# Optimization experiments

Measured on AMD Instinct MI355X. Metric: run time of the kernel, lower is better.

Reference implementation:

```python
import jax, jax.numpy as jnp
import numpy as np

N_NODES = 50000
N_EDGES = 800000
D_IN = 128
D_HID = 128
D_OUT = 2


def setup_inputs() -> dict:
    key = jax.random.key(0)
    ks = jax.random.split(key, 8)
    x = jax.random.normal(ks[0], (N_NODES, D_IN), dtype=jnp.float32)
    edge_index = jax.random.randint(ks[1], (2, N_EDGES), 0, N_NODES, dtype=jnp.int64)
    s = 0.05
    W1_l = jax.random.normal(ks[2], (D_HID, D_IN), dtype=jnp.float32) * s
    W1_r = jax.random.normal(ks[3], (D_HID, D_IN), dtype=jnp.float32) * s
    b1 = jax.random.normal(ks[4], (D_HID,), dtype=jnp.float32) * s
    W2_l = jax.random.normal(ks[5], (D_OUT, D_HID), dtype=jnp.float32) * s
    W2_r = jax.random.normal(ks[6], (D_OUT, D_HID), dtype=jnp.float32) * s
    b2 = jax.random.normal(ks[7], (D_OUT,), dtype=jnp.float32) * s
    return {"x": x, "edge_index": edge_index, "W1_l": W1_l, "W1_r": W1_r,
            "b1": b1, "W2_l": W2_l, "W2_r": W2_r, "b2": b2}


def _sage_conv(x, src, dst, W_l, W_r, b):
    # mean-aggregate neighbor features: gather from src, scatter-sum to dst
    n = x.shape[0]
    msg = x[src]                                            # [E, d]
    agg = jax.ops.segment_sum(msg, dst, num_segments=n)      # [n, d]
    cnt = jax.ops.segment_sum(jnp.ones((src.shape[0],), x.dtype), dst,
                              num_segments=n)
    agg = agg / jnp.maximum(cnt, 1.0)[:, None]
    # lin_l(aggregated) + lin_r(self) + bias  (PyG SAGEConv with root_weight)
    return agg @ W_l.T + x @ W_r.T + b


def reference(x, edge_index, W1_l, W1_r, b1, W2_l, W2_r, b2):
    src, dst = edge_index[0], edge_index[1]
    h = _sage_conv(x, src, dst, W1_l, W1_r, b1)
    h = jax.nn.relu(h)
    out = _sage_conv(h, src, dst, W2_l, W2_r, b2)
    return out
```

## Files before the change

kernel.cpp:

```cpp
#include <hip/hip_runtime.h>

#define N_NODES 50000
#define N_EDGES 800000

typedef __bf16 bf16_8 __attribute__((ext_vector_type(8)));
typedef float  f32_4  __attribute__((ext_vector_type(4)));


__global__ void prep_deg_kernel(const float* __restrict__ W1l, const float* __restrict__ W1r,
                                __bf16* __restrict__ Wt, const float* __restrict__ x,
                                __bf16* __restrict__ xb, const int* __restrict__ dst,
                                int* __restrict__ deg_p, int* __restrict__ edge_pos) {
    int b = blockIdx.x;
    if (b < 3125) {
        int t = b * 256 + threadIdx.x;
        int d = dst[t];
        int pos = atomicAdd(&deg_p[d * 16], 1);
        int node = t >> 4, c8 = t & 15;
        const float4* xp = (const float4*)(x + node * 128 + c8 * 8);
        float4 v0 = xp[0], v1 = xp[1];
        bf16_8 o;
        o[0] = (__bf16)v0.x; o[1] = (__bf16)v0.y; o[2] = (__bf16)v0.z; o[3] = (__bf16)v0.w;
        o[4] = (__bf16)v1.x; o[5] = (__bf16)v1.y; o[6] = (__bf16)v1.z; o[7] = (__bf16)v1.w;
        *(bf16_8*)(xb + t * 8) = o;
        edge_pos[t] = pos;
    } else {
        int t = (b - 3125) * 256 + threadIdx.x;
        int n = t >> 8, k = t & 255;
        float v = (k < 128) ? W1l[n * 128 + k] : W1r[n * 128 + (k - 128)];
        Wt[t] = (__bf16)v;
    }
}

__global__ void scan_block_kernel(const int* __restrict__ deg_p, int* __restrict__ rowptr,
                                  int* __restrict__ degc, int* __restrict__ bsum) {
    __shared__ int s[256];
    int i = blockIdx.x * 256 + threadIdx.x;
    int v = (i < N_NODES) ? deg_p[i * 16] : 0;
    if (i < N_NODES) degc[i] = v;
    s[threadIdx.x] = v;
    __syncthreads();
    #pragma unroll
    for (int off = 1; off < 256; off <<= 1) {
        int t = (threadIdx.x >= off) ? s[threadIdx.x - off] : 0;
        __syncthreads();
        s[threadIdx.x] += t;
        __syncthreads();
    }
    if (i < N_NODES) rowptr[i] = s[threadIdx.x] - v;
    if (threadIdx.x == 255) bsum[blockIdx.x] = s[255];
}

__global__ void scan_bsum_kernel(const int* __restrict__ bsum, int* __restrict__ boff) {
    __shared__ int s[256];
    int tid = threadIdx.x;
    int v = (tid < 196) ? bsum[tid] : 0;
    s[tid] = v;
    __syncthreads();
    #pragma unroll
    for (int off = 1; off < 256; off <<= 1) {
        int t = (tid >= off) ? s[tid - off] : 0;
        __syncthreads();
        s[tid] += t;
        __syncthreads();
    }
    boff[tid] = s[tid] - v;
}

__global__ void fill_csr_kernel(const int* __restrict__ src, const int* __restrict__ dst,
                                const int* __restrict__ rowptr, const int* __restrict__ boff,
                                const int* __restrict__ edge_pos, int* __restrict__ csr) {
    int e = blockIdx.x * 256 + threadIdx.x;
    int d = dst[e];
    csr[rowptr[d] + boff[d >> 8] + edge_pos[e]] = src[e];
}

#define LDA 264
__global__ __launch_bounds__(256) void gather_gemm_kernel(
    const int* __restrict__ rowptr, const int* __restrict__ boff,
    const int* __restrict__ degc, const int* __restrict__ csr,
    const __bf16* __restrict__ xb, const __bf16* __restrict__ Wt,
    const float* __restrict__ b1, const float* __restrict__ W2l,
    const float* __restrict__ W2r, float* __restrict__ y, float* __restrict__ z)
{
    __shared__ __bf16 As[16 * LDA];
    __shared__ float4 sp[4][16];

    const int i0 = blockIdx.x * 16;
    const int tid = threadIdx.x;
    const int row = tid >> 4, c8 = tid & 15;
    const int gi = i0 + row;

    bf16_8 sv = *(const bf16_8*)(xb + gi * 128 + c8 * 8);
    *(bf16_8*)(&As[row * LDA + 128 + c8 * 8]) = sv;

    {
        int beg = rowptr[gi] + boff[gi >> 8];
        int n = degc[gi];
        float acc[8] = {};
        int j = 0;
        for (; j + 8 <= n; j += 8) {
            int idx[8];
            #pragma unroll
            for (int u = 0; u < 8; ++u) idx[u] = csr[beg + j + u];
            bf16_8 vv[8];
            #pragma unroll
            for (int u = 0; u < 8; ++u)
                vv[u] = *(const bf16_8*)(xb + idx[u] * 128 + c8 * 8);
            #pragma unroll
            for (int u = 0; u < 8; ++u) {
                float s01 = (float)vv[0][u] + (float)vv[1][u];
                float s23 = (float)vv[2][u] + (float)vv[3][u];
                float s45 = (float)vv[4][u] + (float)vv[5][u];
                float s67 = (float)vv[6][u] + (float)vv[7][u];
                acc[u] += (s01 + s23) + (s45 + s67);
            }
        }
        for (; j + 2 <= n; j += 2) {
            int s0 = csr[beg + j], s1 = csr[beg + j + 1];
            bf16_8 v0 = *(const bf16_8*)(xb + s0 * 128 + c8 * 8);
            bf16_8 v1 = *(const bf16_8*)(xb + s1 * 128 + c8 * 8);
            #pragma unroll
            for (int u = 0; u < 8; ++u) acc[u] += (float)v0[u] + (float)v1[u];
        }
        if (j < n) {
            int s0 = csr[beg + j];
            bf16_8 v0 = *(const bf16_8*)(xb + s0 * 128 + c8 * 8);
            #pragma unroll
            for (int u = 0; u < 8; ++u) acc[u] += (float)v0[u];
        }
        float inv = 1.0f / fmaxf((float)n, 1.0f);
        bf16_8 o;
        #pragma unroll
        for (int u = 0; u < 8; ++u) o[u] = (__bf16)(acc[u] * inv);
        *(bf16_8*)(&As[row * LDA + c8 * 8]) = o;
    }
    __syncthreads();

    const int wv = tid >> 6, lane = tid & 63;
    const int mr = lane & 15, q = lane >> 4;
    const int n0 = wv * 2, n1 = wv * 2 + 1;

    f32_4 acc0 = (f32_4){0.f,0.f,0.f,0.f}, acc1 = (f32_4){0.f,0.f,0.f,0.f};
    #pragma unroll
    for (int ks = 0; ks < 8; ++ks) {
        bf16_8 a  = *(const bf16_8*)(&As[mr * LDA + ks * 32 + q * 8]);
        bf16_8 b0 = *(const bf16_8*)(Wt + (n0 * 16 + mr) * 256 + ks * 32 + q * 8);
        bf16_8 bb = *(const bf16_8*)(Wt + (n1 * 16 + mr) * 256 + ks * 32 + q * 8);
        acc0 = __builtin_amdgcn_mfma_f32_16x16x32_bf16(a, b0, acc0, 0, 0, 0);
        acc1 = __builtin_amdgcn_mfma_f32_16x16x32_bf16(a, bb, acc1, 0, 0, 0);
    }

    float py0[4] = {}, py1[4] = {}, pz0[4] = {}, pz1[4] = {};
    #pragma unroll
    for (int ntl = 0; ntl < 2; ++ntl) {
        int col = (wv * 2 + ntl) * 16 + mr;
        f32_4 a = ntl ? acc1 : acc0;
        float bb  = b1[col];
        float wl0 = W2l[col], wl1 = W2l[128 + col];
        float wr0 = W2r[col], wr1 = W2r[128 + col];
        #pragma unroll
        for (int r = 0; r < 4; ++r) {
            float hv = fmaxf(a[r] + bb, 0.f);
            py0[r] += hv * wl0; py1[r] += hv * wl1;
            pz0[r] += hv * wr0; pz1[r] += hv * wr1;
        }
    }
    #pragma unroll
    for (int off = 1; off < 16; off <<= 1) {
        #pragma unroll
        for (int r = 0; r < 4; ++r) {
            py0[r] += __shfl_xor(py0[r], off);
            py1[r] += __shfl_xor(py1[r], off);
            pz0[r] += __shfl_xor(pz0[r], off);
            pz1[r] += __shfl_xor(pz1[r], off);
        }
    }
    if (mr < 4) {
        int r = mr;
        sp[wv][q * 4 + r] = make_float4(py0[r], py1[r], pz0[r], pz1[r]);
    }
    __syncthreads();

    if (tid < 16) {
        float4 a0 = sp[0][tid], a1 = sp[1][tid], a2 = sp[2][tid], a3 = sp[3][tid];
        ((float2*)y)[i0 + tid] = make_float2(a0.x + a1.x + a2.x + a3.x,
                                             a0.y + a1.y + a2.y + a3.y);
        ((float2*)z)[i0 + tid] = make_float2(a0.z + a1.z + a2.z + a3.z,
                                             a0.w + a1.w + a2.w + a3.w);
    }
}

__global__ void final_kernel(const int* __restrict__ rowptr, const int* __restrict__ boff,
                             const int* __restrict__ degc, const int* __restrict__ csr,
                             const float* __restrict__ y, const float* __restrict__ z,
                             const float* __restrict__ b2, float* __restrict__ out) {
    int t = blockIdx.x * 256 + threadIdx.x;
    int node = t >> 2, p = t & 3;
    if (node >= N_NODES) return;
    int beg = rowptr[node] + boff[node >> 8], n = degc[node];
    float a0 = 0.f, a1 = 0.f;
    for (int j = p; j < n; j += 4) {
        float2 v = ((const float2*)y)[csr[beg + j]];
        a0 += v.x; a1 += v.y;
    }
    a0 += __shfl_xor(a0, 1); a1 += __shfl_xor(a1, 1);
    a0 += __shfl_xor(a0, 2); a1 += __shfl_xor(a1, 2);
    if (p == 0) {
        float inv = 1.0f / fmaxf((float)n, 1.0f);
        float2 zz = ((const float2*)z)[node];
        ((float2*)out)[node] = make_float2(a0 * inv + zz.x + b2[0],
                                           a1 * inv + zz.y + b2[1]);
    }
}

extern "C" void kernel_launch(void* const* d_in, const int* in_sizes, int n_in,
                              void* d_out, int out_size, void* d_ws, size_t ws_size,
                              hipStream_t stream) {
    const float* x   = (const float*)d_in[0];
    const int*   ei  = (const int*)  d_in[1];
    const float* W1l = (const float*)d_in[2];
    const float* W1r = (const float*)d_in[3];
    const float* b1  = (const float*)d_in[4];
    const float* W2l = (const float*)d_in[5];
    const float* W2r = (const float*)d_in[6];
    const float* b2  = (const float*)d_in[7];
    float* out = (float*)d_out;
    const int* src = ei;
    const int* dst = ei + N_EDGES;

    char* ws = (char*)d_ws;
    int*    deg_p    = (int*)   (ws + 0);
    int*    boff     = (int*)   (ws + 0);
    int*    edge_pos = (int*)   (ws + 3200000);
    int*    rowptr   = (int*)   (ws + 6400000);
    int*    degc     = (int*)   (ws + 6600192);
    int*    bsum     = (int*)   (ws + 6800384);
    int*    csr      = (int*)   (ws + 6801408);
    __bf16* xb       = (__bf16*)(ws + 10001408);
    float*  y        = (float*) (ws + 35601408);
    float*  z        = (float*) (ws + 36001408);
    __bf16* Wt       = (__bf16*)(ws + 36401408);

    hipMemsetAsync(deg_p, 0, 3200000, stream);
    prep_deg_kernel<<<3253, 256, 0, stream>>>(W1l, W1r, Wt, x, xb, dst, deg_p, edge_pos);
    scan_block_kernel<<<196, 256, 0, stream>>>(deg_p, rowptr, degc, bsum);
    scan_bsum_kernel<<<1, 256, 0, stream>>>(bsum, boff);
    fill_csr_kernel<<<3125, 256, 0, stream>>>(src, dst, rowptr, boff, edge_pos, csr);
    gather_gemm_kernel<<<3125, 256, 0, stream>>>(rowptr, boff, degc, csr, xb, Wt, b1, W2l, W2r, y, z);
    final_kernel<<<782, 256, 0, stream>>>(rowptr, boff, degc, csr, y, z, b2, out);
}
```

Before: 189.7 us.

## Split neighbor gathers across two threads per chunk and widen final aggregation

Measured after the change: 204.3 us. +7.7%, slower.

```diff
diff --git a/kernel.cpp b/kernel.cpp
--- a/kernel.cpp
+++ b/kernel.cpp
@@ -76,7 +76,7 @@
 }
 
 #define LDA 264
-__global__ __launch_bounds__(256) void gather_gemm_kernel(
+__global__ __launch_bounds__(512) void gather_gemm_kernel(
     const int* __restrict__ rowptr, const int* __restrict__ boff,
     const int* __restrict__ degc, const int* __restrict__ csr,
     const __bf16* __restrict__ xb, const __bf16* __restrict__ Wt,
@@ -84,25 +84,30 @@
     const float* __restrict__ W2r, float* __restrict__ y, float* __restrict__ z)
 {
     __shared__ __bf16 As[16 * LDA];
-    __shared__ float4 sp[4][16];
+    __shared__ float4 sp[8][16];
 
     const int i0 = blockIdx.x * 16;
     const int tid = threadIdx.x;
-    const int row = tid >> 4, c8 = tid & 15;
-    const int gi = i0 + row;
-
-    bf16_8 sv = *(const bf16_8*)(xb + gi * 128 + c8 * 8);
-    *(bf16_8*)(&As[row * LDA + 128 + c8 * 8]) = sv;
+
+    if (tid < 256) {
+        int r = tid >> 4, cc = tid & 15;
+        *(bf16_8*)(&As[r * LDA + 128 + cc * 8]) =
+            *(const bf16_8*)(xb + (i0 + r) * 128 + cc * 8);
+    }
 
     {
+        const int row = tid >> 5, c8 = (tid >> 1) & 15, half = tid & 1;
+        const int gi = i0 + row;
         int beg = rowptr[gi] + boff[gi >> 8];
         int n = degc[gi];
+        int m = (n - half + 1) >> 1;
+        const int* cp = csr + beg + half;
         float acc[8] = {};
-        int j = 0;
-        for (; j + 8 <= n; j += 8) {
+        int k = 0;
+        for (; k + 8 <= m; k += 8) {
             int idx[8];
             #pragma unroll
-            for (int u = 0; u < 8; ++u) idx[u] = csr[beg + j + u];
+            for (int u = 0; u < 8; ++u) idx[u] = cp[2 * (k + u)];
             bf16_8 vv[8];
             #pragma unroll
             for (int u = 0; u < 8; ++u)
@@ -116,52 +121,66 @@
                 acc[u] += (s01 + s23) + (s45 + s67);
             }
         }
-        for (; j + 2 <= n; j += 2) {
-            int s0 = csr[beg + j], s1 = csr[beg + j + 1];
-            bf16_8 v0 = *(const bf16_8*)(xb + s0 * 128 + c8 * 8);
-            bf16_8 v1 = *(const bf16_8*)(xb + s1 * 128 + c8 * 8);
+        if (k + 4 <= m) {
+            int idx[4];
+            #pragma unroll
+            for (int u = 0; u < 4; ++u) idx[u] = cp[2 * (k + u)];
+            bf16_8 vv[4];
+            #pragma unroll
+            for (int u = 0; u < 4; ++u)
+                vv[u] = *(const bf16_8*)(xb + idx[u] * 128 + c8 * 8);
+            #pragma unroll
+            for (int u = 0; u < 8; ++u)
+                acc[u] += ((float)vv[0][u] + (float)vv[1][u]) +
+                          ((float)vv[2][u] + (float)vv[3][u]);
+            k += 4;
+        }
+        if (k + 2 <= m) {
+            int i0e = cp[2 * k], i1e = cp[2 * k + 2];
+            bf16_8 v0 = *(const bf16_8*)(xb + i0e * 128 + c8 * 8);
+            bf16_8 v1 = *(const bf16_8*)(xb + i1e * 128 + c8 * 8);
             #pragma unroll
             for (int u = 0; u < 8; ++u) acc[u] += (float)v0[u] + (float)v1[u];
-        }
-        if (j < n) {
-            int s0 = csr[beg + j];
-            bf16_8 v0 = *(const bf16_8*)(xb + s0 * 128 + c8 * 8);
+            k += 2;
+        }
+        if (k < m) {
+            int i0e = cp[2 * k];
+            bf16_8 v0 = *(const bf16_8*)(xb + i0e * 128 + c8 * 8);
             #pragma unroll
             for (int u = 0; u < 8; ++u) acc[u] += (float)v0[u];
         }
-        float inv = 1.0f / fmaxf((float)n, 1.0f);
-        bf16_8 o;
-        #pragma unroll
-        for (int u = 0; u < 8; ++u) o[u] = (__bf16)(acc[u] * inv);
-        *(bf16_8*)(&As[row * LDA + c8 * 8]) = o;
+        #pragma unroll
+        for (int u = 0; u < 8; ++u) acc[u] += __shfl_xor(acc[u], 1);
+        if (half == 0) {
+            float inv = 1.0f / fmaxf((float)n, 1.0f);
+            bf16_8 o;
+            #pragma unroll
+            for (int u = 0; u < 8; ++u) o[u] = (__bf16)(acc[u] * inv);
+            *(bf16_8*)(&As[row * LDA + c8 * 8]) = o;
+        }
     }
     __syncthreads();
 
     const int wv = tid >> 6, lane = tid & 63;
     const int mr = lane & 15, q = lane >> 4;
-    const int n0 = wv * 2, n1 = wv * 2 + 1;
-
-    f32_4 acc0 = (f32_4){0.f,0.f,0.f,0.f}, acc1 = (f32_4){0.f,0.f,0.f,0.f};
+
+    f32_4 acc0 = (f32_4){0.f,0.f,0.f,0.f};
     #pragma unroll
     for (int ks = 0; ks < 8; ++ks) {
-        bf16_8 a  = *(const bf16_8*)(&As[mr * LDA + ks * 32 + q * 8]);
-        bf16_8 b0 = *(const bf16_8*)(Wt + (n0 * 16 + mr) * 256 + ks * 32 + q * 8);
-        bf16_8 bb = *(const bf16_8*)(Wt + (n1 * 16 + mr) * 256 + ks * 32 + q * 8);
-        acc0 = __builtin_amdgcn_mfma_f32_16x16x32_bf16(a, b0, acc0, 0, 0, 0);
-        acc1 = __builtin_amdgcn_mfma_f32_16x16x32_bf16(a, bb, acc1, 0, 0, 0);
+        bf16_8 a = *(const bf16_8*)(&As[mr * LDA + ks * 32 + q * 8]);
+        bf16_8 b = *(const bf16_8*)(Wt + (wv * 16 + mr) * 256 + ks * 32 + q * 8);
+        acc0 = __builtin_amdgcn_mfma_f32_16x16x32_bf16(a, b, acc0, 0, 0, 0);
     }
 
     float py0[4] = {}, py1[4] = {}, pz0[4] = {}, pz1[4] = {};
-    #pragma unroll
-    for (int ntl = 0; ntl < 2; ++ntl) {
-        int col = (wv * 2 + ntl) * 16 + mr;
-        f32_4 a = ntl ? acc1 : acc0;
+    {
+        int col = wv * 16 + mr;
         float bb  = b1[col];
         float wl0 = W2l[col], wl1 = W2l[128 + col];
         float wr0 = W2r[col], wr1 = W2r[128 + col];
         #pragma unroll
         for (int r = 0; r < 4; ++r) {
-            float hv = fmaxf(a[r] + bb, 0.f);
+            float hv = fmaxf(acc0[r] + bb, 0.f);
             py0[r] += hv * wl0; py1[r] += hv * wl1;
             pz0[r] += hv * wr0; pz1[r] += hv * wr1;
         }
@@ -183,11 +202,14 @@
     __syncthreads();
 
     if (tid < 16) {
-        float4 a0 = sp[0][tid], a1 = sp[1][tid], a2 = sp[2][tid], a3 = sp[3][tid];
-        ((float2*)y)[i0 + tid] = make_float2(a0.x + a1.x + a2.x + a3.x,
-                                             a0.y + a1.y + a2.y + a3.y);
-        ((float2*)z)[i0 + tid] = make_float2(a0.z + a1.z + a2.z + a3.z,
-                                             a0.w + a1.w + a2.w + a3.w);
+        float s0 = 0.f, s1 = 0.f, s2 = 0.f, s3 = 0.f;
+        #pragma unroll
+        for (int w = 0; w < 8; ++w) {
+            float4 a = sp[w][tid];
+            s0 += a.x; s1 += a.y; s2 += a.z; s3 += a.w;
+        }
+        ((float2*)y)[i0 + tid] = make_float2(s0, s1);
+        ((float2*)z)[i0 + tid] = make_float2(s2, s3);
     }
 }
 
@@ -196,16 +218,17 @@
                              const float* __restrict__ y, const float* __restrict__ z,
                              const float* __restrict__ b2, float* __restrict__ out) {
     int t = blockIdx.x * 256 + threadIdx.x;
-    int node = t >> 2, p = t & 3;
+    int node = t >> 3, p = t & 7;
     if (node >= N_NODES) return;
     int beg = rowptr[node] + boff[node >> 8], n = degc[node];
     float a0 = 0.f, a1 = 0.f;
-    for (int j = p; j < n; j += 4) {
+    for (int j = p; j < n; j += 8) {
         float2 v = ((const float2*)y)[csr[beg + j]];
         a0 += v.x; a1 += v.y;
     }
     a0 += __shfl_xor(a0, 1); a1 += __shfl_xor(a1, 1);
     a0 += __shfl_xor(a0, 2); a1 += __shfl_xor(a1, 2);
+    a0 += __shfl_xor(a0, 4); a1 += __shfl_xor(a1, 4);
     if (p == 0) {
         float inv = 1.0f / fmaxf((float)n, 1.0f);
         float2 zz = ((const float2*)z)[node];
@@ -247,6 +270,6 @@
     scan_block_kernel<<<196, 256, 0, stream>>>(deg_p, rowptr, degc, bsum);
     scan_bsum_kernel<<<1, 256, 0, stream>>>(bsum, boff);
     fill_csr_kernel<<<3125, 256, 0, stream>>>(src, dst, rowptr, boff, edge_pos, csr);
-    gather_gemm_kernel<<<3125, 256, 0, stream>>>(rowptr, boff, degc, csr, xb, Wt, b1, W2l, W2r, y, z);
-    final_kernel<<<782, 256, 0, stream>>>(rowptr, boff, degc, csr, y, z, b2, out);
-}
+    gather_gemm_kernel<<<3125, 512, 0, stream>>>(rowptr, boff, degc, csr, xb, Wt, b1, W2l, W2r, y, z);
+    final_kernel<<<1563, 256, 0, stream>>>(rowptr, boff, degc, csr, y, z, b2, out);
+}
```
